# Performance work log

Measured on AMD Instinct MI355X. Metric: run time of the kernel, lower is better.

The kernel has to match this reference:

```python
import jax, jax.numpy as jnp
import numpy as np

N_NODES = 50000


def _gcn_norm(edge_index, num_nodes):
    # Add self-loops (PyG GCNConv default) and compute symmetric norm.
    loops = jnp.arange(num_nodes, dtype=edge_index.dtype)
    src = jnp.concatenate([edge_index[0], loops])
    dst = jnp.concatenate([edge_index[1], loops])
    ones = jnp.ones(src.shape[0], dtype=jnp.float32)
    deg = jax.ops.segment_sum(ones, dst, num_segments=num_nodes)
    deg_inv_sqrt = jnp.where(deg > 0, jax.lax.rsqrt(jnp.maximum(deg, 1.0)), 0.0)
    norm = deg_inv_sqrt[src] * deg_inv_sqrt[dst]  # [E + N]
    return src, dst, norm


def _gcn_conv(x, src, dst, norm, W, b, num_nodes):
    xw = x @ W                               # [N, out]
    msg = xw[src] * norm[:, None]            # gather + scale  [E+N, out]
    out = jax.ops.segment_sum(msg, dst, num_segments=num_nodes)  # scatter-add
    return out + b


def setup_inputs() -> dict:
    key = jax.random.key(0)
    ks = jax.random.split(key, 10)
    d_in, d_h, d_out = 64, 64, 8
    n_edges = 800000
    x = jax.random.normal(ks[0], (N_NODES, d_in), dtype=jnp.float32)
    edge_index = jax.random.randint(ks[1], (2, n_edges), 0, N_NODES, dtype=jnp.int64)
    def w(k, fan_in, fan_out):
        return jax.random.normal(k, (fan_in, fan_out), dtype=jnp.float32) * (1.0 / np.sqrt(fan_in))
    return {
        "x": x,
        "edge_index": edge_index,
        "W0": w(ks[2], d_in, d_h), "b0": jnp.zeros((d_h,), jnp.float32),
        "W1": w(ks[3], d_h, d_h), "b1": jnp.zeros((d_h,), jnp.float32),
        "W2": w(ks[4], d_h, d_h), "b2": jnp.zeros((d_h,), jnp.float32),
        "linW": w(ks[5], d_h, d_out), "linb": jnp.zeros((d_out,), jnp.float32),
    }


def reference(x, edge_index, W0, b0, W1, b1, W2, b2, linW, linb):
    num_nodes = x.shape[0]
    src, dst, norm = _gcn_norm(edge_index, num_nodes)
    # 3 GCNConv layers, ReLU; dropout is identity at inference (training=False).
    for W, b in ((W0, b0), (W1, b1), (W2, b2)):
        x = jax.nn.relu(_gcn_conv(x, src, dst, norm, W, b, num_nodes))
    return x @ linW + linb
```

## Files before the change

kernel.cpp:

```cpp
#include <hip/hip_runtime.h>
#include <hip/hip_fp16.h>

#define TPB 256
#define CAP 16384
#define CAPSH 14
#define SC_BLOCKS 256

typedef __attribute__((ext_vector_type(8))) float f32x8;
typedef __attribute__((ext_vector_type(8))) unsigned short u16x8;
typedef __attribute__((ext_vector_type(4))) unsigned int u32x4;
typedef __attribute__((ext_vector_type(2))) _Float16 h16x2;


__device__ __forceinline__ int ld_idx(const void* p, long long i, int is64) {
    return is64 ? (int)((const long long*)p)[i] : ((const int*)p)[i];
}

__device__ __forceinline__ ushort4 f4_to_h4(float4 v) {
    ushort4 r;
    r.x = __half_as_ushort(__float2half_rn(v.x));
    r.y = __half_as_ushort(__float2half_rn(v.y));
    r.z = __half_as_ushort(__float2half_rn(v.z));
    r.w = __half_as_ushort(__float2half_rn(v.w));
    return r;
}

__global__ __launch_bounds__(TPB) void p3_scatter(const void* __restrict__ ei,
                                                  long long E,
                                                  int* __restrict__ gcur,
                                                  int* __restrict__ pairs) {
    __shared__ int cnt[TPB];
    __shared__ int cur2[TPB];
    __shared__ int s_is64;
    int t = threadIdx.x;
    if (t < 64) {
        const unsigned int* w = (const unsigned int*)ei;
        unsigned long long m = __ballot(w[2 * t + 1] != 0u);
        if (t == 0) s_is64 = (m == 0ull) ? 1 : 0;
    }
    cnt[t] = 0;
    __syncthreads();
    const int is64 = s_is64;
    long long chunk = (E + SC_BLOCKS - 1) / SC_BLOCKS;
    long long s0 = (long long)blockIdx.x * chunk;
    long long s1 = (s0 + chunk < E) ? s0 + chunk : E;

    for (long long e = s0 + t; e < s1; e += TPB) {
        int d = ld_idx(ei, E + e, is64);
        atomicAdd(&cnt[d >> 8], 1);
    }
    __syncthreads();
    if (cnt[t]) cur2[t] = (t << CAPSH) + atomicAdd(&gcur[t], cnt[t]);
    __syncthreads();
    for (long long e = s0 + t; e < s1; e += TPB) {
        int sv = ld_idx(ei, e, is64);
        int d  = ld_idx(ei, E + e, is64);
        int pos = atomicAdd(&cur2[d >> 8], 1);
        pairs[pos] = (sv << 8) | (d & 255);
    }
}

__global__ __launch_bounds__(TPB) void p4_fill(const int* __restrict__ pairs,
                                               const int* __restrict__ gcur,
                                               const float* __restrict__ x,
                                               int2* __restrict__ meta,
                                               int* __restrict__ csr,
                                               ushort4* __restrict__ z0, int N) {
    __shared__ int ldeg[TPB];
    __shared__ int ssc[TPB];
    __shared__ int cur[TPB];
    __shared__ float fdis[TPB];
    int t = threadIdx.x;
    int b = blockIdx.x;
    int base = b << CAPSH;
    int ecnt = gcur[b];
    ldeg[t] = 0;
    __syncthreads();
    for (int e = base + t; e < base + ecnt; e += TPB)
        atomicAdd(&ldeg[pairs[e] & 255], 1);
    __syncthreads();
    int dv = ldeg[t];
    int pv = (dv + 7) & ~7;
    ssc[t] = pv;
    __syncthreads();
    for (int off = 1; off < TPB; off <<= 1) {
        int u = 0;
        if (t >= off) u = ssc[t - off];
        __syncthreads();
        ssc[t] += u;
        __syncthreads();
    }
    int o = base + ssc[t] - pv;
    cur[t] = o;
    float dd = rsqrtf((float)(dv + 1));
    fdis[t] = dd;
    int node = (b << 8) + t;
    if (node < N)
        meta[node] = make_int2((o << 8) | (pv >> 3), __float_as_int(dd));
    __syncthreads();
    for (int e = base + t; e < base + ecnt; e += TPB) {
        int p = pairs[e];
        int pos = atomicAdd(&cur[p & 255], 1);
        csr[pos] = p >> 8;
    }
    for (int e = o + dv; e < o + pv; ++e) csr[e] = N;

    int ni = t >> 4, c = t & 15;
    for (int p = 0; p < 16; ++p) {
        int nd = (b << 8) + p * 16 + ni;
        if (nd < N) {
            float dvv = fdis[p * 16 + ni];
            float4 h = ((const float4*)x)[(size_t)nd * 16 + c];
            float4 r = {h.x * dvv, h.y * dvv, h.z * dvv, h.w * dvv};
            z0[(size_t)nd * 16 + c] = f4_to_h4(r);
        }
    }
    if (b == 0 && t < 16) z0[(size_t)N * 16 + t] = make_ushort4(0, 0, 0, 0);
}


#if __has_builtin(__builtin_amdgcn_fdot2) && __has_builtin(__builtin_amdgcn_perm)
#define GCN_DOT2 1
#else
#define GCN_DOT2 0
#endif

__device__ __forceinline__ void accum_row_pair(const u16x8& ra, const u16x8& rb,
                                               f32x8& acc) {
#if GCN_DOT2
    u32x4 a = __builtin_bit_cast(u32x4, ra);
    u32x4 b = __builtin_bit_cast(u32x4, rb);
    const h16x2 one = {(_Float16)1.0f, (_Float16)1.0f};
    #pragma unroll
    for (int j = 0; j < 4; ++j) {
        unsigned p0 = __builtin_amdgcn_perm(a[j], b[j], 0x05040100u);
        unsigned p1 = __builtin_amdgcn_perm(a[j], b[j], 0x07060302u);
        acc[2 * j]     = __builtin_amdgcn_fdot2(__builtin_bit_cast(h16x2, p0),
                                                one, acc[2 * j], false);
        acc[2 * j + 1] = __builtin_amdgcn_fdot2(__builtin_bit_cast(h16x2, p1),
                                                one, acc[2 * j + 1], false);
    }
#else
    #pragma unroll
    for (int i = 0; i < 8; ++i)
        acc[i] += __half2float(__ushort_as_half(ra[i])) +
                  __half2float(__ushort_as_half(rb[i]));
#endif
}

__device__ __forceinline__ void accum_batch(const u16x8 (&R)[8], f32x8& acc) {
    #pragma unroll
    for (int k = 0; k < 8; k += 2) accum_row_pair(R[k], R[k + 1], acc);
}

__device__ __forceinline__ void load_batch(const u16x8* __restrict__ z8,
                                           u16x8 (&R)[8], int idx, int c,
                                           int base) {
    #pragma unroll
    for (int k = 0; k < 8; ++k) {
        int s = __shfl(idx, base + k);
        R[k] = z8[(size_t)s * 8 + c];
    }
}

__device__ __forceinline__ f32x8 gather_rows(const u16x8* __restrict__ z8,
                                             const int* __restrict__ csr,
                                             int start, int nbatch, int c,
                                             f32x8 acc) {
    const int base = threadIdx.x & 56;
    if (nbatch <= 0) return acc;
    u16x8 A[8], B[8];
    int idx0 = csr[start + c];
    int idx_n = (nbatch > 1) ? csr[start + 8 + c] : 0;
    load_batch(z8, A, idx0, c, base);
    int bt = 0;
    for (;;) {
        int idx_f = (bt + 2 < nbatch) ? csr[start + (bt + 2) * 8 + c] : 0;
        if (bt + 1 < nbatch) load_batch(z8, B, idx_n, c, base);
        accum_batch(A, acc);
        if (++bt >= nbatch) break;
        int idx_f2 = (bt + 2 < nbatch) ? csr[start + (bt + 2) * 8 + c] : 0;
        if (bt + 1 < nbatch) load_batch(z8, A, idx_f, c, base);
        accum_batch(B, acc);
        if (++bt >= nbatch) break;
        idx_n = idx_f2;
    }
    return acc;
}

__device__ __forceinline__ f32x8 shfl_mm8(f32x8 s, const float4* Ws4, int c) {
    const int base = threadIdx.x & 56;
    f32x8 u = {0.f, 0.f, 0.f, 0.f, 0.f, 0.f, 0.f, 0.f};
    #pragma unroll
    for (int q = 0; q < 8; ++q) {
        #pragma unroll
        for (int r = 0; r < 8; ++r) {
            float hv = __shfl(s[r], base + q);
            float4 w0 = Ws4[(q * 8 + r) * 16 + 2 * c];
            float4 w1 = Ws4[(q * 8 + r) * 16 + 2 * c + 1];
            u[0] = fmaf(hv, w0.x, u[0]);
            u[1] = fmaf(hv, w0.y, u[1]);
            u[2] = fmaf(hv, w0.z, u[2]);
            u[3] = fmaf(hv, w0.w, u[3]);
            u[4] = fmaf(hv, w1.x, u[4]);
            u[5] = fmaf(hv, w1.y, u[5]);
            u[6] = fmaf(hv, w1.z, u[6]);
            u[7] = fmaf(hv, w1.w, u[7]);
        }
    }
    return u;
}

__device__ __forceinline__ u16x8 f8_to_h8(f32x8 v) {
    u16x8 r;
    #pragma unroll
    for (int i = 0; i < 8; ++i)
        r[i] = __half_as_ushort(__float2half_rn(v[i]));
    return r;
}

__global__ __launch_bounds__(TPB) void layer_mm(const u16x8* __restrict__ z,
                                                const int* __restrict__ csr,
                                                const int2* __restrict__ meta,
                                                const float* __restrict__ b,
                                                const float* __restrict__ W,
                                                u16x8* __restrict__ zout, int n) {
    __shared__ float Ws[64 * 64];
    int t = threadIdx.x;
    float4* Ws4 = (float4*)Ws;
    const float4* W4g = (const float4*)W;
    #pragma unroll
    for (int i = 0; i < 4; ++i) Ws4[t + i * TPB] = W4g[t + i * TPB];

    if (blockIdx.x == 0 && t < 8) {
        u16x8 zz = {0, 0, 0, 0, 0, 0, 0, 0};
        zout[(size_t)n * 8 + t] = zz;
    }

    int wave = t >> 6, lane = t & 63;
    int g = lane >> 3, c = lane & 7;
    int node = blockIdx.x * 32 + wave * 8 + g;
    f32x8 s = {0.f, 0.f, 0.f, 0.f, 0.f, 0.f, 0.f, 0.f};
    float dv = 0.f;
    if (node < n) {
        int2 m = meta[node];
        int start = ((unsigned)m.x) >> 8;
        int nbatch = m.x & 255;
        dv = __int_as_float(m.y);
        u16x8 v = z[(size_t)node * 8 + c];
        #pragma unroll
        for (int i = 0; i < 8; ++i) s[i] = __half2float(__ushort_as_half(v[i]));
        s = gather_rows(z, csr, start, nbatch, c, s);
    }
    __syncthreads();
    f32x8 u = shfl_mm8(s, Ws4, c);
    if (node < n) {
        float4 b0 = ((const float4*)b)[2 * c];
        float4 b1 = ((const float4*)b)[2 * c + 1];
        f32x8 r;
        r[0] = fmaxf(fmaf(dv, u[0], b0.x), 0.f) * dv;
        r[1] = fmaxf(fmaf(dv, u[1], b0.y), 0.f) * dv;
        r[2] = fmaxf(fmaf(dv, u[2], b0.z), 0.f) * dv;
        r[3] = fmaxf(fmaf(dv, u[3], b0.w), 0.f) * dv;
        r[4] = fmaxf(fmaf(dv, u[4], b1.x), 0.f) * dv;
        r[5] = fmaxf(fmaf(dv, u[5], b1.y), 0.f) * dv;
        r[6] = fmaxf(fmaf(dv, u[6], b1.z), 0.f) * dv;
        r[7] = fmaxf(fmaf(dv, u[7], b1.w), 0.f) * dv;
        zout[(size_t)node * 8 + c] = f8_to_h8(r);
    }
}

__global__ __launch_bounds__(TPB) void layer_final(const u16x8* __restrict__ z,
                                                   const int* __restrict__ csr,
                                                   const int2* __restrict__ meta,
                                                   const float* __restrict__ b,
                                                   const float* __restrict__ W,
                                                   const float* __restrict__ Wl,
                                                   const float* __restrict__ bl,
                                                   float* __restrict__ out, int n) {
    __shared__ float Ws[64 * 64];
    __shared__ float Wls[64 * 8];
    __shared__ float bls[8];
    int t = threadIdx.x;
    float4* Ws4 = (float4*)Ws;
    const float4* W4g = (const float4*)W;
    #pragma unroll
    for (int i = 0; i < 4; ++i) Ws4[t + i * TPB] = W4g[t + i * TPB];
    if (t < 128) ((float4*)Wls)[t] = ((const float4*)Wl)[t];
    if (t < 8) bls[t] = bl[t];

    int wave = t >> 6, lane = t & 63;
    int g = lane >> 3, c = lane & 7;
    int node = blockIdx.x * 32 + wave * 8 + g;
    f32x8 s = {0.f, 0.f, 0.f, 0.f, 0.f, 0.f, 0.f, 0.f};
    float dv = 0.f;
    if (node < n) {
        int2 m = meta[node];
        int start = ((unsigned)m.x) >> 8;
        int nbatch = m.x & 255;
        dv = __int_as_float(m.y);
        u16x8 v = z[(size_t)node * 8 + c];
        #pragma unroll
        for (int i = 0; i < 8; ++i) s[i] = __half2float(__ushort_as_half(v[i]));
        s = gather_rows(z, csr, start, nbatch, c, s);
    }
    __syncthreads();
    f32x8 u = shfl_mm8(s, Ws4, c);
    float4 b0 = ((const float4*)b)[2 * c];
    float4 b1 = ((const float4*)b)[2 * c + 1];
    f32x8 h;
    h[0] = fmaxf(fmaf(dv, u[0], b0.x), 0.f);
    h[1] = fmaxf(fmaf(dv, u[1], b0.y), 0.f);
    h[2] = fmaxf(fmaf(dv, u[2], b0.z), 0.f);
    h[3] = fmaxf(fmaf(dv, u[3], b0.w), 0.f);
    h[4] = fmaxf(fmaf(dv, u[4], b1.x), 0.f);
    h[5] = fmaxf(fmaf(dv, u[5], b1.y), 0.f);
    h[6] = fmaxf(fmaf(dv, u[6], b1.z), 0.f);
    h[7] = fmaxf(fmaf(dv, u[7], b1.w), 0.f);

    const int base = threadIdx.x & 56;
    float acc = bls[c];
    #pragma unroll
    for (int q = 0; q < 8; ++q) {
        #pragma unroll
        for (int r = 0; r < 8; ++r) {
            float hv = __shfl(h[r], base + q);
            acc = fmaf(hv, Wls[(q * 8 + r) * 8 + c], acc);
        }
    }
    if (node < n) out[(size_t)node * 8 + c] = acc;
}

extern "C" void kernel_launch(void* const* d_in, const int* in_sizes, int n_in,
                              void* d_out, int out_size, void* d_ws, size_t ws_size,
                              hipStream_t stream) {
    const float* x  = (const float*)d_in[0];
    const void*  ei = d_in[1];
    const float* W0 = (const float*)d_in[2];
    const float* b0 = (const float*)d_in[3];
    const float* W1 = (const float*)d_in[4];
    const float* b1 = (const float*)d_in[5];
    const float* W2 = (const float*)d_in[6];
    const float* b2 = (const float*)d_in[7];
    const float* Wl = (const float*)d_in[8];
    const float* bl = (const float*)d_in[9];

    const long long E = in_sizes[1] / 2;
    const int dh = in_sizes[3];
    const int din = in_sizes[2] / dh;
    const int N = in_sizes[0] / din;
    const int nb = (N + 255) >> 8;

    char* ws = (char*)d_ws;
    size_t off = 0;
    auto alloc = [&](size_t bytes) -> char* {
        char* r = ws + off;
        off += (bytes + 255) & ~(size_t)255;
        return r;
    };
    int*   gcur    = (int*)  alloc(1024);
    int2*  meta    = (int2*) alloc((size_t)N * 8);
    int*   pairs   = (int*)  alloc((size_t)nb * CAP * 4);
    int*   csr     = (int*)  alloc((size_t)nb * CAP * 4);
    u16x8* zbA     = (u16x8*)alloc((size_t)(N + 1) * 64 * 2);
    u16x8* zbB     = (u16x8*)alloc((size_t)(N + 1) * 64 * 2);

    hipMemsetAsync(gcur, 0, 256 * sizeof(int), stream);
    p3_scatter<<<SC_BLOCKS, TPB, 0, stream>>>(ei, E, gcur, pairs);
    p4_fill<<<nb, TPB, 0, stream>>>(pairs, gcur, x, meta, csr,
                                    (ushort4*)zbA, N);

    const int gL = (N + 31) / 32;
    layer_mm<<<gL, TPB, 0, stream>>>(zbA, csr, meta, b0, W0, zbB, N);
    layer_mm<<<gL, TPB, 0, stream>>>(zbB, csr, meta, b1, W1, zbA, N);
    layer_final<<<gL, TPB, 0, stream>>>(zbA, csr, meta, b2, W2, Wl, bl,
                                        (float*)d_out, N);
}
```

Baseline: 186.6 us.

## Use MFMA 16x16x32 f16 for per-layer dense transform with 16-node wave tiles

```diff
diff --git a/kernel.cpp b/kernel.cpp
--- a/kernel.cpp
+++ b/kernel.cpp
@@ -10,6 +10,8 @@
 typedef __attribute__((ext_vector_type(8))) unsigned short u16x8;
 typedef __attribute__((ext_vector_type(4))) unsigned int u32x4;
 typedef __attribute__((ext_vector_type(2))) _Float16 h16x2;
+typedef __attribute__((ext_vector_type(8))) _Float16 h16x8;
+typedef __attribute__((ext_vector_type(4))) float f32x4;
 
 
 __device__ __forceinline__ int ld_idx(const void* p, long long i, int is64) {
@@ -148,78 +150,52 @@
 #endif
 }
 
-__device__ __forceinline__ void accum_batch(const u16x8 (&R)[8], f32x8& acc) {
-    #pragma unroll
-    for (int k = 0; k < 8; k += 2) accum_row_pair(R[k], R[k + 1], acc);
-}
-
-__device__ __forceinline__ void load_batch(const u16x8* __restrict__ z8,
-                                           u16x8 (&R)[8], int idx, int c,
-                                           int base) {
-    #pragma unroll
-    for (int k = 0; k < 8; ++k) {
-        int s = __shfl(idx, base + k);
-        R[k] = z8[(size_t)s * 8 + c];
-    }
-}
-
-__device__ __forceinline__ f32x8 gather_rows(const u16x8* __restrict__ z8,
-                                             const int* __restrict__ csr,
-                                             int start, int nbatch, int c,
-                                             f32x8 acc) {
-    const int base = threadIdx.x & 56;
-    if (nbatch <= 0) return acc;
-    u16x8 A[8], B[8];
-    int idx0 = csr[start + c];
-    int idx_n = (nbatch > 1) ? csr[start + 8 + c] : 0;
-    load_batch(z8, A, idx0, c, base);
-    int bt = 0;
-    for (;;) {
-        int idx_f = (bt + 2 < nbatch) ? csr[start + (bt + 2) * 8 + c] : 0;
-        if (bt + 1 < nbatch) load_batch(z8, B, idx_n, c, base);
-        accum_batch(A, acc);
-        if (++bt >= nbatch) break;
-        int idx_f2 = (bt + 2 < nbatch) ? csr[start + (bt + 2) * 8 + c] : 0;
-        if (bt + 1 < nbatch) load_batch(z8, A, idx_f, c, base);
-        accum_batch(B, acc);
-        if (++bt >= nbatch) break;
-        idx_n = idx_f2;
-    }
-    return acc;
-}
-
-__device__ __forceinline__ f32x8 shfl_mm8(f32x8 s, const float4* Ws4, int c) {
-    const int base = threadIdx.x & 56;
-    f32x8 u = {0.f, 0.f, 0.f, 0.f, 0.f, 0.f, 0.f, 0.f};
-    #pragma unroll
-    for (int q = 0; q < 8; ++q) {
-        #pragma unroll
-        for (int r = 0; r < 8; ++r) {
-            float hv = __shfl(s[r], base + q);
-            float4 w0 = Ws4[(q * 8 + r) * 16 + 2 * c];
-            float4 w1 = Ws4[(q * 8 + r) * 16 + 2 * c + 1];
-            u[0] = fmaf(hv, w0.x, u[0]);
-            u[1] = fmaf(hv, w0.y, u[1]);
-            u[2] = fmaf(hv, w0.z, u[2]);
-            u[3] = fmaf(hv, w0.w, u[3]);
-            u[4] = fmaf(hv, w1.x, u[4]);
-            u[5] = fmaf(hv, w1.y, u[5]);
-            u[6] = fmaf(hv, w1.z, u[6]);
-            u[7] = fmaf(hv, w1.w, u[7]);
-        }
-    }
-    return u;
-}
-
-__device__ __forceinline__ u16x8 f8_to_h8(f32x8 v) {
-    u16x8 r;
-    #pragma unroll
-    for (int i = 0; i < 8; ++i)
-        r[i] = __half_as_ushort(__float2half_rn(v[i]));
-    return r;
-}
-
-__global__ __launch_bounds__(TPB) void layer_mm(const u16x8* __restrict__ z,
+__device__ __forceinline__ void gather_mfma(const u16x8* __restrict__ z,
+                                            const int* __restrict__ csr,
+                                            int start, int nbatch, int q, int r,
+                                            f32x8& lo, f32x8& hi) {
+    const int2* csr2 = (const int2*)csr;
+    int ib = (start >> 1) + q;
+    int2 ip = (nbatch > 0) ? csr2[ib] : make_int2(0, 0);
+    for (int bt = 0; bt < nbatch; ++bt) {
+        int2 ipn = (bt + 1 < nbatch) ? csr2[ib + (bt + 1) * 4] : make_int2(0, 0);
+        int s0 = __shfl(ip.x, r);
+        int s1 = __shfl(ip.y, r);
+        int s2 = __shfl(ip.x, r + 16);
+        int s3 = __shfl(ip.y, r + 16);
+        int s4 = __shfl(ip.x, r + 32);
+        int s5 = __shfl(ip.y, r + 32);
+        int s6 = __shfl(ip.x, r + 48);
+        int s7 = __shfl(ip.y, r + 48);
+        u16x8 l0 = z[(size_t)s0 * 8 + q], h0 = z[(size_t)s0 * 8 + 4 + q];
+        u16x8 l1 = z[(size_t)s1 * 8 + q], h1 = z[(size_t)s1 * 8 + 4 + q];
+        u16x8 l2 = z[(size_t)s2 * 8 + q], h2 = z[(size_t)s2 * 8 + 4 + q];
+        u16x8 l3 = z[(size_t)s3 * 8 + q], h3 = z[(size_t)s3 * 8 + 4 + q];
+        u16x8 l4 = z[(size_t)s4 * 8 + q], h4 = z[(size_t)s4 * 8 + 4 + q];
+        u16x8 l5 = z[(size_t)s5 * 8 + q], h5 = z[(size_t)s5 * 8 + 4 + q];
+        u16x8 l6 = z[(size_t)s6 * 8 + q], h6 = z[(size_t)s6 * 8 + 4 + q];
+        u16x8 l7 = z[(size_t)s7 * 8 + q], h7 = z[(size_t)s7 * 8 + 4 + q];
+        accum_row_pair(l0, l1, lo); accum_row_pair(h0, h1, hi);
+        accum_row_pair(l2, l3, lo); accum_row_pair(h2, h3, hi);
+        accum_row_pair(l4, l5, lo); accum_row_pair(h4, h5, hi);
+        accum_row_pair(l6, l7, lo); accum_row_pair(h6, h7, hi);
+        ip = ipn;
+    }
+}
+
+__device__ __forceinline__ void build_wfrags(const float* __restrict__ Ws,
+                                             int q, int r, h16x8 wf[4][2]) {
+    #pragma unroll
+    for (int jt = 0; jt < 4; ++jt)
+        #pragma unroll
+        for (int ks = 0; ks < 2; ++ks)
+            #pragma unroll
+            for (int i = 0; i < 8; ++i)
+                wf[jt][ks][i] =
+                    (_Float16)Ws[(ks * 32 + q * 8 + i) * 64 + jt * 16 + r];
+}
+
+__global__ __launch_bounds__(TPB, 4) void layer_mm(const u16x8* __restrict__ z,
                                                 const int* __restrict__ csr,
                                                 const int2* __restrict__ meta,
                                                 const float* __restrict__ b,
@@ -238,39 +214,65 @@
     }
 
     int wave = t >> 6, lane = t & 63;
-    int g = lane >> 3, c = lane & 7;
-    int node = blockIdx.x * 32 + wave * 8 + g;
-    f32x8 s = {0.f, 0.f, 0.f, 0.f, 0.f, 0.f, 0.f, 0.f};
-    float dv = 0.f;
+    int q = lane >> 4, r = lane & 15;
+    int base = blockIdx.x * 64 + wave * 16;
+    int node = base + r;
+    f32x8 lo = {0.f, 0.f, 0.f, 0.f, 0.f, 0.f, 0.f, 0.f};
+    f32x8 hi = {0.f, 0.f, 0.f, 0.f, 0.f, 0.f, 0.f, 0.f};
+    int start = 0, nbatch = 0;
     if (node < n) {
         int2 m = meta[node];
-        int start = ((unsigned)m.x) >> 8;
-        int nbatch = m.x & 255;
-        dv = __int_as_float(m.y);
-        u16x8 v = z[(size_t)node * 8 + c];
-        #pragma unroll
-        for (int i = 0; i < 8; ++i) s[i] = __half2float(__ushort_as_half(v[i]));
-        s = gather_rows(z, csr, start, nbatch, c, s);
-    }
-    __syncthreads();
-    f32x8 u = shfl_mm8(s, Ws4, c);
-    if (node < n) {
-        float4 b0 = ((const float4*)b)[2 * c];
-        float4 b1 = ((const float4*)b)[2 * c + 1];
-        f32x8 r;
-        r[0] = fmaxf(fmaf(dv, u[0], b0.x), 0.f) * dv;
-        r[1] = fmaxf(fmaf(dv, u[1], b0.y), 0.f) * dv;
-        r[2] = fmaxf(fmaf(dv, u[2], b0.z), 0.f) * dv;
-        r[3] = fmaxf(fmaf(dv, u[3], b0.w), 0.f) * dv;
-        r[4] = fmaxf(fmaf(dv, u[4], b1.x), 0.f) * dv;
-        r[5] = fmaxf(fmaf(dv, u[5], b1.y), 0.f) * dv;
-        r[6] = fmaxf(fmaf(dv, u[6], b1.z), 0.f) * dv;
-        r[7] = fmaxf(fmaf(dv, u[7], b1.w), 0.f) * dv;
-        zout[(size_t)node * 8 + c] = f8_to_h8(r);
-    }
-}
-
-__global__ __launch_bounds__(TPB) void layer_final(const u16x8* __restrict__ z,
+        start = ((unsigned)m.x) >> 8;
+        nbatch = m.x & 255;
+        u16x8 v0 = z[(size_t)node * 8 + q];
+        u16x8 v1 = z[(size_t)node * 8 + 4 + q];
+        #pragma unroll
+        for (int i = 0; i < 8; ++i) {
+            lo[i] = __half2float(__ushort_as_half(v0[i]));
+            hi[i] = __half2float(__ushort_as_half(v1[i]));
+        }
+    }
+    gather_mfma(z, csr, start, nbatch, q, r, lo, hi);
+    __syncthreads();
+
+    h16x8 wf[4][2];
+    build_wfrags(Ws, q, r, wf);
+    h16x8 a0, a1;
+    #pragma unroll
+    for (int i = 0; i < 8; ++i) {
+        a0[i] = (_Float16)lo[i];
+        a1[i] = (_Float16)hi[i];
+    }
+    f32x4 zero4 = {0.f, 0.f, 0.f, 0.f};
+    f32x4 acc[4] = {zero4, zero4, zero4, zero4};
+    #pragma unroll
+    for (int jt = 0; jt < 4; ++jt) {
+        acc[jt] = __builtin_amdgcn_mfma_f32_16x16x32_f16(a0, wf[jt][0], acc[jt], 0, 0, 0);
+        acc[jt] = __builtin_amdgcn_mfma_f32_16x16x32_f16(a1, wf[jt][1], acc[jt], 0, 0, 0);
+    }
+
+    float dvv[4];
+    #pragma unroll
+    for (int i = 0; i < 4; ++i) {
+        int nd = base + q * 4 + i;
+        dvv[i] = (nd < n) ? __int_as_float(meta[nd].y) : 0.f;
+    }
+    #pragma unroll
+    for (int jt = 0; jt < 4; ++jt) {
+        float bv = b[jt * 16 + r];
+        #pragma unroll
+        for (int i = 0; i < 4; ++i) {
+            int nd = base + q * 4 + i;
+            if (nd < n) {
+                float val = fmaxf(fmaf(dvv[i], acc[jt][i], bv), 0.f) * dvv[i];
+                ((unsigned short*)zout)[(size_t)nd * 64 + jt * 16 + r] =
+                    __half_as_ushort(__float2half_rn(val));
+            }
+        }
+    }
+}
+
+__global__ __launch_bounds__(TPB, 4) void layer_final(const u16x8* __restrict__ z,
                                                    const int* __restrict__ csr,
                                                    const int2* __restrict__ meta,
                                                    const float* __restrict__ b,
@@ -281,6 +283,7 @@
     __shared__ float Ws[64 * 64];
     __shared__ float Wls[64 * 8];
     __shared__ float bls[8];
+    __shared__ __align__(16) _Float16 hbuf[4][16][64];
     int t = threadIdx.x;
     float4* Ws4 = (float4*)Ws;
     const float4* W4g = (const float4*)W;
@@ -290,45 +293,79 @@
     if (t < 8) bls[t] = bl[t];
 
     int wave = t >> 6, lane = t & 63;
-    int g = lane >> 3, c = lane & 7;
-    int node = blockIdx.x * 32 + wave * 8 + g;
-    f32x8 s = {0.f, 0.f, 0.f, 0.f, 0.f, 0.f, 0.f, 0.f};
-    float dv = 0.f;
+    int q = lane >> 4, r = lane & 15;
+    int base = blockIdx.x * 64 + wave * 16;
+    int node = base + r;
+    f32x8 lo = {0.f, 0.f, 0.f, 0.f, 0.f, 0.f, 0.f, 0.f};
+    f32x8 hi = {0.f, 0.f, 0.f, 0.f, 0.f, 0.f, 0.f, 0.f};
+    int start = 0, nbatch = 0;
     if (node < n) {
         int2 m = meta[node];
-        int start = ((unsigned)m.x) >> 8;
-        int nbatch = m.x & 255;
-        dv = __int_as_float(m.y);
-        u16x8 v = z[(size_t)node * 8 + c];
-        #pragma unroll
-        for (int i = 0; i < 8; ++i) s[i] = __half2float(__ushort_as_half(v[i]));
-        s = gather_rows(z, csr, start, nbatch, c, s);
-    }
-    __syncthreads();
-    f32x8 u = shfl_mm8(s, Ws4, c);
-    float4 b0 = ((const float4*)b)[2 * c];
-    float4 b1 = ((const float4*)b)[2 * c + 1];
-    f32x8 h;
-    h[0] = fmaxf(fmaf(dv, u[0], b0.x), 0.f);
-    h[1] = fmaxf(fmaf(dv, u[1], b0.y), 0.f);
-    h[2] = fmaxf(fmaf(dv, u[2], b0.z), 0.f);
-    h[3] = fmaxf(fmaf(dv, u[3], b0.w), 0.f);
-    h[4] = fmaxf(fmaf(dv, u[4], b1.x), 0.f);
-    h[5] = fmaxf(fmaf(dv, u[5], b1.y), 0.f);
-    h[6] = fmaxf(fmaf(dv, u[6], b1.z), 0.f);
-    h[7] = fmaxf(fmaf(dv, u[7], b1.w), 0.f);
-
-    const int base = threadIdx.x & 56;
-    float acc = bls[c];
-    #pragma unroll
-    for (int q = 0; q < 8; ++q) {
-        #pragma unroll
-        for (int r = 0; r < 8; ++r) {
-            float hv = __shfl(h[r], base + q);
-            acc = fmaf(hv, Wls[(q * 8 + r) * 8 + c], acc);
-        }
-    }
-    if (node < n) out[(size_t)node * 8 + c] = acc;
+        start = ((unsigned)m.x) >> 8;
+        nbatch = m.x & 255;
+        u16x8 v0 = z[(size_t)node * 8 + q];
+        u16x8 v1 = z[(size_t)node * 8 + 4 + q];
+        #pragma unroll
+        for (int i = 0; i < 8; ++i) {
+            lo[i] = __half2float(__ushort_as_half(v0[i]));
+            hi[i] = __half2float(__ushort_as_half(v1[i]));
+        }
+    }
+    gather_mfma(z, csr, start, nbatch, q, r, lo, hi);
+    __syncthreads();
+
+    h16x8 wf[4][2];
+    build_wfrags(Ws, q, r, wf);
+    h16x8 a0, a1;
+    #pragma unroll
+    for (int i = 0; i < 8; ++i) {
+        a0[i] = (_Float16)lo[i];
+        a1[i] = (_Float16)hi[i];
+    }
+    f32x4 zero4 = {0.f, 0.f, 0.f, 0.f};
+    f32x4 acc[4] = {zero4, zero4, zero4, zero4};
+    #pragma unroll
+    for (int jt = 0; jt < 4; ++jt) {
+        acc[jt] = __builtin_amdgcn_mfma_f32_16x16x32_f16(a0, wf[jt][0], acc[jt], 0, 0, 0);
+        acc[jt] = __builtin_amdgcn_mfma_f32_16x16x32_f16(a1, wf[jt][1], acc[jt], 0, 0, 0);
+    }
+
+    float dvv[4];
+    #pragma unroll
+    for (int i = 0; i < 4; ++i) {
+        int nd = base + q * 4 + i;
+        dvv[i] = (nd < n) ? __int_as_float(meta[nd].y) : 0.f;
+    }
+    #pragma unroll
+    for (int jt = 0; jt < 4; ++jt) {
+        float bv = b[jt * 16 + r];
+        #pragma unroll
+        for (int i = 0; i < 4; ++i) {
+            float hv = fmaxf(fmaf(dvv[i], acc[jt][i], bv), 0.f);
+            hbuf[wave][q * 4 + i][jt * 16 + r] = (_Float16)hv;
+        }
+    }
+
+    h16x8 wl2[2];
+    #pragma unroll
+    for (int ks = 0; ks < 2; ++ks)
+        #pragma unroll
+        for (int i = 0; i < 8; ++i)
+            wl2[ks][i] = (r < 8) ? (_Float16)Wls[(ks * 32 + q * 8 + i) * 8 + r]
+                                 : (_Float16)0.f;
+    h16x8 a20 = *(const h16x8*)&hbuf[wave][r][q * 8];
+    h16x8 a21 = *(const h16x8*)&hbuf[wave][r][32 + q * 8];
+    f32x4 acc2 = zero4;
+    acc2 = __builtin_amdgcn_mfma_f32_16x16x32_f16(a20, wl2[0], acc2, 0, 0, 0);
+    acc2 = __builtin_amdgcn_mfma_f32_16x16x32_f16(a21, wl2[1], acc2, 0, 0, 0);
+    if (r < 8) {
+        float blv = bls[r];
+        #pragma unroll
+        for (int i = 0; i < 4; ++i) {
+            int nd = base + q * 4 + i;
+            if (nd < n) out[(size_t)nd * 8 + r] = acc2[i] + blv;
+        }
+    }
 }
 
 extern "C" void kernel_launch(void* const* d_in, const int* in_sizes, int n_in,
@@ -370,7 +407,7 @@
     p4_fill<<<nb, TPB, 0, stream>>>(pairs, gcur, x, meta, csr,
                                     (ushort4*)zbA, N);
 
-    const int gL = (N + 31) / 32;
+    const int gL = (N + 63) / 64;
     layer_mm<<<gL, TPB, 0, stream>>>(zbA, csr, meta, b0, W0, zbB, N);
     layer_mm<<<gL, TPB, 0, stream>>>(zbB, csr, meta, b1, W1, zbA, N);
     layer_final<<<gL, TPB, 0, stream>>>(zbA, csr, meta, b2, W2, Wl, bl,
```

Measured after the change: 192.5 us. 1.03x slower.
